# Kernel optimization log

Measured on AMD Instinct MI355X. Metric: run time of the kernel, lower is better.

Reference implementation:

```python
import jax, jax.numpy as jnp
import numpy as np

N, E, IN, H, G = 100000, 1600000, 64, 108, 128
N_LAYERS = 2  # hidden_dims=[108,108] -> 1 layer from hidden_dims[1:] + 1 final layer


def setup_inputs() -> dict:
    key = jax.random.key(0)
    ks = jax.random.split(key, 13)
    s = lambda fan_in: 1.0 / np.sqrt(fan_in)
    inp = {
        "nodes_feat": jax.random.normal(ks[0], (N, IN), jnp.float32),
        "edges_feat": jax.random.normal(ks[1], (E, 1), jnp.float32),
        "nodes_num_norm_sqrt": jax.random.uniform(ks[2], (N,), jnp.float32),
        "edges_num_norm_sqrt": jax.random.uniform(ks[3], (E,), jnp.float32),
        "W_emb": jax.random.uniform(ks[4], (IN, H), jnp.float32, -s(IN), s(IN)),
        "b_emb": jax.random.uniform(ks[5], (H,), jnp.float32, -s(IN), s(IN)),
        "pool_W": jax.random.uniform(ks[6], (N_LAYERS, H, H), jnp.float32, -s(H), s(H)),
        "pool_b": jax.random.uniform(ks[7], (N_LAYERS, H), jnp.float32, -s(H), s(H)),
        "app_W": jax.random.uniform(ks[8], (N_LAYERS, 2 * H, H), jnp.float32, -s(2 * H), s(2 * H)),
        "app_b": jax.random.uniform(ks[9], (N_LAYERS, H), jnp.float32, -s(2 * H), s(2 * H)),
        "src": jax.random.randint(ks[10], (E,), 0, N, jnp.int64 if jax.config.jax_enable_x64 else jnp.int32),
        "dst": jax.random.randint(ks[11], (E,), 0, N, jnp.int64 if jax.config.jax_enable_x64 else jnp.int32),
        "graph_ids": jnp.sort(jax.random.randint(ks[12], (N,), 0, G, jnp.int64 if jax.config.jax_enable_x64 else jnp.int32)),
        "n_graphs": G,
    }
    return inp


def reference(nodes_feat, edges_feat, nodes_num_norm_sqrt, edges_num_norm_sqrt,
              W_emb, b_emb, pool_W, pool_b, app_W, app_b,
              src, dst, graph_ids, n_graphs):
    n = nodes_feat.shape[0]
    # embedding_h
    h = nodes_feat @ W_emb + b_emb  # [N, H]
    # in-degree for mean aggregation (dropout = 0.0 so omitted)
    deg = jax.ops.segment_sum(jnp.ones((src.shape[0],), h.dtype), dst, num_segments=n)
    deg = jnp.maximum(deg, 1.0)[:, None]  # [N, 1]
    for i in range(pool_W.shape[0]):
        h_in = h
        # meanpool aggregator: per-message linear+ReLU == per-node transform then gather
        z = jax.nn.relu(h @ pool_W[i] + pool_b[i])  # [N, H]
        c = jax.ops.segment_sum(z[src], dst, num_segments=n) / deg  # mean over neighbors
        # NodeApply: linear(concat(h, c)) -> L2 normalize -> activation
        b = jnp.concatenate([h, c], axis=1) @ app_W[i] + app_b[i]
        b = b / jnp.maximum(jnp.linalg.norm(b, axis=1, keepdims=True), 1e-12)
        h = h_in + jax.nn.relu(b)  # residual (dims match: 108 == 108)
    # dgl.mean_nodes readout per graph
    cnt = jax.ops.segment_sum(jnp.ones((n,), h.dtype), graph_ids, num_segments=n_graphs)
    hg = jax.ops.segment_sum(h, graph_ids, num_segments=n_graphs) / jnp.maximum(cnt, 1.0)[:, None]
    return hg  # [n_graphs, H]
```

## Files before the change

kernel.cpp:

```cpp
#include <hip/hip_runtime.h>

#define HDIM 108
constexpr int G_GRAPHS = 128;
constexpr int MAXNB = 1024;
constexpr int CAP = 2560;

typedef _Float16 half8 __attribute__((ext_vector_type(8)));
typedef _Float16 half4v __attribute__((ext_vector_type(4)));
typedef float floatx4 __attribute__((ext_vector_type(4)));
typedef float floatx2 __attribute__((ext_vector_type(2)));

__device__ inline unsigned char f32_to_fp8(float t) {
#if __has_builtin(__builtin_amdgcn_cvt_pk_fp8_f32)
  return (unsigned char)(__builtin_amdgcn_cvt_pk_fp8_f32(t, t, 0, false) & 0xFF);
#else
  t = fminf(t, 448.f);
  if (t < 0.015625f) return (unsigned char)__float2int_rn(t * 512.f);
  unsigned u = __float_as_uint(t);
  unsigned lsb = (u >> 20) & 1;
  u += 0x7FFFFu + lsb;
  int e = (int)((u >> 23) & 0xFF) - 127;
  if (e > 8) return 0x7E;
  return (unsigned char)(((e + 7) << 3) | ((u >> 20) & 7));
#endif
}

template <bool HI>
__device__ inline floatx2 fp8x2_to_f32(unsigned v) {
#if __has_builtin(__builtin_amdgcn_cvt_pk_f32_fp8)
  return __builtin_amdgcn_cvt_pk_f32_fp8((int)v, HI);
#else
  unsigned b0 = HI ? ((v >> 16) & 0xFF) : (v & 0xFF);
  unsigned b1 = HI ? ((v >> 24) & 0xFF) : ((v >> 8) & 0xFF);
  floatx2 r;
  {
    unsigned s = b0 >> 7, e = (b0 >> 3) & 0xF, m = b0 & 7;
    float f = (e == 0) ? (float)m * 0.001953125f
                       : __uint_as_float(((e + 120u) << 23) | (m << 20));
    r[0] = s ? -f : f;
  }
  {
    unsigned s = b1 >> 7, e = (b1 >> 3) & 0xF, m = b1 & 7;
    float f = (e == 0) ? (float)m * 0.001953125f
                       : __uint_as_float(((e + 120u) << 23) | (m << 20));
    r[1] = s ? -f : f;
  }
  return r;
#endif
}

__global__ __launch_bounds__(256) void k_cvtall(const float* __restrict__ W_emb,
                                                const float* __restrict__ pool_W,
                                                const float* __restrict__ app_W,
                                                _Float16* __restrict__ wte,
                                                _Float16* __restrict__ wtp,
                                                _Float16* __restrict__ wta) {
  int idx = blockIdx.x * 256 + threadIdx.x;
  if (idx >= 86016) return;
  const float* src;
  _Float16* dst;
  int Kpad, K, split, rel;
  if (idx < 7168)       { rel = idx;          src = W_emb;            dst = wte;              Kpad = 64;  K = 64;  split = 0; }
  else if (idx < 21504) { rel = idx - 7168;   src = pool_W;           dst = wtp;              Kpad = 128; K = 108; split = 0; }
  else if (idx < 35840) { rel = idx - 21504;  src = pool_W + 11664;   dst = wtp + 14336;      Kpad = 128; K = 108; split = 0; }
  else if (idx < 60928) { rel = idx - 35840;  src = app_W;            dst = wta;              Kpad = 224; K = 216; split = 1; }
  else                  { rel = idx - 60928;  src = app_W + 23328;    dst = wta + 25088;      Kpad = 224; K = 216; split = 1; }
  int n = rel / Kpad, k = rel - n * Kpad;
  int ks;
  if (split) ks = (k < 108) ? k : (k >= 112 && k < 220) ? (k - 4) : -1;
  else       ks = (k < K) ? k : -1;
  float v = (n < 108 && ks >= 0) ? src[ks * 108 + n] : 0.f;
  dst[rel] = (_Float16)v;
}

__global__ __launch_bounds__(1024) void k_scatter(const int* __restrict__ src, const int* __restrict__ dst,
                                                  int* __restrict__ gcur, int* __restrict__ ebuf,
                                                  int E, int nb) {
  __shared__ int hist[MAXNB];
  const int tid = threadIdx.x;
  const int e0 = blockIdx.x * 16384;
  for (int b = tid; b < nb; b += 1024) hist[b] = 0;
  __syncthreads();
#pragma unroll
  for (int it = 0; it < 16; it++) {
    int e = e0 + it * 1024 + tid;
    if (e < E) atomicAdd(&hist[dst[e] >> 7], 1);
  }
  __syncthreads();
  for (int b = tid; b < nb; b += 1024) {
    int h = hist[b];
    hist[b] = h ? atomicAdd(&gcur[b * 16], h) : 0;
  }
  __syncthreads();
#pragma unroll
  for (int it = 0; it < 16; it++) {
    int e = e0 + it * 1024 + tid;
    if (e < E) {
      int d = dst[e];
      int b = d >> 7;
      int rank = atomicAdd(&hist[b], 1);
      if (rank < CAP) ebuf[(size_t)b * CAP + rank] = src[e] | ((d & 127) << 20);
    }
  }
}

__global__ __launch_bounds__(1024) void k_bagg(const unsigned char* __restrict__ z, const int* __restrict__ ebuf,
                                               const int* __restrict__ gcur, _Float16* __restrict__ c16,
                                               int N, int nb) {
  __shared__ int cnts[128];
  __shared__ int scanb[128];
  __shared__ int off[129];
  __shared__ int ecur[128];
  __shared__ int esrc[CAP];
  const int tid = threadIdx.x;
  const int b = blockIdx.x;
  const int v0 = b << 7;
  int cntb = gcur[b * 16];
  if (cntb > CAP) cntb = CAP;
  const int* eb = ebuf + (size_t)b * CAP;

  if (tid < 128) cnts[tid] = 0;
  __syncthreads();
  for (int i = tid; i < cntb; i += 1024) atomicAdd(&cnts[eb[i] >> 20], 1);
  __syncthreads();
  if (tid < 128) scanb[tid] = cnts[tid];
  __syncthreads();
#pragma unroll
  for (int st = 1; st < 128; st <<= 1) {
    int v = 0;
    if (tid < 128 && tid >= st) v = scanb[tid - st];
    __syncthreads();
    if (tid < 128) scanb[tid] += v;
    __syncthreads();
  }
  if (tid == 0) off[0] = 0;
  if (tid < 128) {
    off[tid + 1] = scanb[tid];
    ecur[tid] = scanb[tid] - cnts[tid];
  }
  __syncthreads();
  for (int i = tid; i < cntb; i += 1024) {
    int e = eb[i];
    int p = atomicAdd(&ecur[e >> 20], 1);
    esrc[p] = e & 0xFFFFF;
  }
  __syncthreads();

  const int lane = tid & 31;
  const int grp = tid >> 5;
  if (lane >= 28) return;
  const unsigned char* __restrict__ zl = z + lane * 4;
#pragma unroll 1
  for (int r = grp; r < 128; r += 32) {
    int v = v0 + r;
    if (v >= N) continue;
    int s = off[r], e2 = off[r + 1];
    float a0 = 0.f, a1 = 0.f, a2 = 0.f, a3 = 0.f;
    int j = s;
    for (; j + 4 <= e2; j += 4) {
      unsigned q0 = *(const unsigned*)(zl + (size_t)esrc[j] * 112);
      unsigned q1 = *(const unsigned*)(zl + (size_t)esrc[j + 1] * 112);
      unsigned q2 = *(const unsigned*)(zl + (size_t)esrc[j + 2] * 112);
      unsigned q3 = *(const unsigned*)(zl + (size_t)esrc[j + 3] * 112);
      floatx2 l0 = fp8x2_to_f32<false>(q0), h0 = fp8x2_to_f32<true>(q0);
      floatx2 l1 = fp8x2_to_f32<false>(q1), h1 = fp8x2_to_f32<true>(q1);
      floatx2 l2 = fp8x2_to_f32<false>(q2), h2 = fp8x2_to_f32<true>(q2);
      floatx2 l3 = fp8x2_to_f32<false>(q3), h3 = fp8x2_to_f32<true>(q3);
      a0 += (l0[0] + l1[0]) + (l2[0] + l3[0]);
      a1 += (l0[1] + l1[1]) + (l2[1] + l3[1]);
      a2 += (h0[0] + h1[0]) + (h2[0] + h3[0]);
      a3 += (h0[1] + h1[1]) + (h2[1] + h3[1]);
    }
    for (; j < e2; j++) {
      unsigned q0 = *(const unsigned*)(zl + (size_t)esrc[j] * 112);
      floatx2 l0 = fp8x2_to_f32<false>(q0), h0 = fp8x2_to_f32<true>(q0);
      a0 += l0[0]; a1 += l0[1]; a2 += h0[0]; a3 += h0[1];
    }
    int d = e2 - s;
    float inv = 1.f / (float)(d > 0 ? d : 1);
    half4v r4;
    r4[0] = (_Float16)(a0 * inv); r4[1] = (_Float16)(a1 * inv);
    r4[2] = (_Float16)(a2 * inv); r4[3] = (_Float16)(a3 * inv);
    *(half4v*)(c16 + (size_t)v * 112 + lane * 4) = r4;
  }
}

template <int KCH, int MODE>
__global__ __launch_bounds__(256, 2) void k_mmf(const void* Asrc, const _Float16* __restrict__ c16,
                                                const _Float16* __restrict__ Wt, const float* __restrict__ bias,
                                                void* outp, int N) {
  constexpr int KW = KCH * 32;
  __shared__ _Float16 As[128 * 40];
  __shared__ _Float16 Ws[112 * 40];

  const int tid = threadIdx.x;
  const int wave = tid >> 6;
  const int lane = tid & 63;
  const int lo = lane & 15;
  const int quad = lane >> 4;
  const int n0 = blockIdx.x * 128;
  const _Float16* h16 = (const _Float16*)Asrc;
  const float* feat = (const float*)Asrc;

  floatx4 acc[2][7];
#pragma unroll
  for (int rt = 0; rt < 2; rt++)
#pragma unroll
    for (int ct = 0; ct < 7; ct++) {
      floatx4 zz = {0.f, 0.f, 0.f, 0.f};
      acc[rt][ct] = zz;
    }

#pragma unroll 1
  for (int kc = 0; kc < KCH; kc++) {
#pragma unroll
    for (int it = 0; it < 2; it++) {
      int idx = tid + it * 256;
      int r = idx >> 2, sg = idx & 3;
      int gn = n0 + r;
      int k = kc * 32 + sg * 8;
      half8 v = {0, 0, 0, 0, 0, 0, 0, 0};
      if (gn < N) {
        if (MODE == 0) {
          float4 f0 = *(const float4*)(feat + (size_t)gn * 64 + k);
          float4 f1 = *(const float4*)(feat + (size_t)gn * 64 + k + 4);
          v[0] = (_Float16)f0.x; v[1] = (_Float16)f0.y; v[2] = (_Float16)f0.z; v[3] = (_Float16)f0.w;
          v[4] = (_Float16)f1.x; v[5] = (_Float16)f1.y; v[6] = (_Float16)f1.z; v[7] = (_Float16)f1.w;
        } else if (MODE == 2) {
          const _Float16* sp = (k < 112) ? (h16 + (size_t)gn * 112 + k)
                                         : (c16 + (size_t)gn * 112 + (k - 112));
          v = *(const half8*)sp;
        } else {
          if (k < 112) v = *(const half8*)(h16 + (size_t)gn * 112 + k);
        }
      }
      *(half8*)&As[r * 40 + sg * 8] = v;
    }
#pragma unroll
    for (int it = 0; it < 2; it++) {
      int idx = tid + it * 256;
      if (idx < 112 * 4) {
        int nrow = idx >> 2, sg = idx & 3;
        half8 v = *(const half8*)(Wt + (size_t)nrow * KW + kc * 32 + sg * 8);
        *(half8*)&Ws[nrow * 40 + sg * 8] = v;
      }
    }
    __syncthreads();

    half8 a0 = *(const half8*)&As[(wave * 32 + lo) * 40 + quad * 8];
    half8 a1 = *(const half8*)&As[(wave * 32 + 16 + lo) * 40 + quad * 8];
#pragma unroll
    for (int ct = 0; ct < 7; ct++) {
      half8 b = *(const half8*)&Ws[(ct * 16 + lo) * 40 + quad * 8];
      acc[0][ct] = __builtin_amdgcn_mfma_f32_16x16x32_f16(a0, b, acc[0][ct], 0, 0, 0);
      acc[1][ct] = __builtin_amdgcn_mfma_f32_16x16x32_f16(a1, b, acc[1][ct], 0, 0, 0);
    }
    __syncthreads();
  }

  float bias_v[7];
#pragma unroll
  for (int ct = 0; ct < 7; ct++) {
    int col = ct * 16 + lo;
    bias_v[ct] = (col < 108) ? bias[col] : 0.f;
  }

  if (MODE == 2) {
    _Float16* out16 = (_Float16*)outp;
#pragma unroll
    for (int rt = 0; rt < 2; rt++) {
#pragma unroll
      for (int reg = 0; reg < 4; reg++) {
        int gr = n0 + wave * 32 + rt * 16 + quad * 4 + reg;
        float bv[7];
        float ssq = 0.f;
#pragma unroll
        for (int ct = 0; ct < 7; ct++) {
          float t = acc[rt][ct][reg] + bias_v[ct];
          bv[ct] = t;
          ssq += t * t;
        }
#pragma unroll
        for (int s = 1; s < 16; s <<= 1) ssq += __shfl_xor(ssq, s, 16);
        float scale = 1.f / fmaxf(sqrtf(ssq), 1e-12f);
        if (gr < N) {
          _Float16* hp = out16 + (size_t)gr * 112 + lo;
#pragma unroll
          for (int ct = 0; ct < 7; ct++) {
            float hv = (float)hp[ct * 16];
            hp[ct * 16] = (_Float16)(hv + fmaxf(bv[ct] * scale, 0.f));
          }
        }
      }
    }
  } else if (MODE == 1) {
    unsigned char* outb = (unsigned char*)outp;
#pragma unroll
    for (int rt = 0; rt < 2; rt++) {
#pragma unroll
      for (int reg = 0; reg < 4; reg++) {
        int gr = n0 + wave * 32 + rt * 16 + quad * 4 + reg;
        if (gr < N) {
          unsigned char* op = outb + (size_t)gr * 112 + lo;
#pragma unroll
          for (int ct = 0; ct < 7; ct++) {
            float t = fmaxf(acc[rt][ct][reg] + bias_v[ct], 0.f);
            op[ct * 16] = f32_to_fp8(t);
          }
        }
      }
    }
  } else {
    _Float16* out16 = (_Float16*)outp;
#pragma unroll
    for (int rt = 0; rt < 2; rt++) {
#pragma unroll
      for (int reg = 0; reg < 4; reg++) {
        int gr = n0 + wave * 32 + rt * 16 + quad * 4 + reg;
        if (gr < N) {
          _Float16* op = out16 + (size_t)gr * 112 + lo;
#pragma unroll
          for (int ct = 0; ct < 7; ct++) {
            float t = acc[rt][ct][reg] + bias_v[ct];
            op[ct * 16] = (_Float16)t;
          }
        }
      }
    }
  }
}

__global__ __launch_bounds__(256) void k_readout(const _Float16* __restrict__ h, const int* __restrict__ gid,
                                                 float* __restrict__ hg, int N) {
  const int CH = 64;
  const int lane = threadIdx.x & 31;
  const int grp = threadIdx.x >> 5;
  int start = (blockIdx.x * 8 + grp) * CH;
  if (start >= N || lane >= 27) return;
  int end = min(start + CH, N);
  float a0 = 0.f, a1 = 0.f, a2 = 0.f, a3 = 0.f;
  int cur = gid[start];
  for (int i = start; i < end; i++) {
    int g = gid[i];
    if (g != cur) {
      float* base = &hg[(size_t)cur * HDIM + lane * 4];
      atomicAdd(base + 0, a0); atomicAdd(base + 1, a1);
      atomicAdd(base + 2, a2); atomicAdd(base + 3, a3);
      a0 = a1 = a2 = a3 = 0.f;
      cur = g;
    }
    half4v v = *(const half4v*)(h + (size_t)i * 112 + lane * 4);
    a0 += (float)v[0]; a1 += (float)v[1]; a2 += (float)v[2]; a3 += (float)v[3];
  }
  float* base = &hg[(size_t)cur * HDIM + lane * 4];
  atomicAdd(base + 0, a0); atomicAdd(base + 1, a1);
  atomicAdd(base + 2, a2); atomicAdd(base + 3, a3);
}

__global__ __launch_bounds__(256) void k_div(const float* __restrict__ hg, const int* __restrict__ gid,
                                             float* __restrict__ out, int total, int N) {
  int i = blockIdx.x * 256 + threadIdx.x;
  if (i < total) {
    int g = i / HDIM;
    int lo = 0, hi = N;
    while (lo < hi) { int m = (lo + hi) >> 1; if (gid[m] < g) lo = m + 1; else hi = m; }
    int lb = lo;
    lo = 0; hi = N;
    while (lo < hi) { int m = (lo + hi) >> 1; if (gid[m] <= g) lo = m + 1; else hi = m; }
    int c = lo - lb;
    out[i] = hg[i] / (float)(c > 0 ? c : 1);
  }
}

extern "C" void kernel_launch(void* const* d_in, const int* in_sizes, int n_in,
                              void* d_out, int out_size, void* d_ws, size_t ws_size,
                              hipStream_t stream) {
  (void)n_in; (void)ws_size; (void)out_size;
  const float* nodes_feat = (const float*)d_in[0];
  const float* W_emb = (const float*)d_in[4];
  const float* b_emb = (const float*)d_in[5];
  const float* pool_W = (const float*)d_in[6];
  const float* pool_b = (const float*)d_in[7];
  const float* app_W = (const float*)d_in[8];
  const float* app_b = (const float*)d_in[9];
  const int* src = (const int*)d_in[10];
  const int* dst = (const int*)d_in[11];
  const int* gid = (const int*)d_in[12];
  const int N = in_sizes[2];
  const int E = in_sizes[10];
  float* out = (float*)d_out;

  const int nb = (N + 127) >> 7;

  char* ws = (char*)d_ws;
  size_t off = 0;
  auto alloc = [&](size_t bytes) -> size_t {
    size_t o = off;
    off += (bytes + 1023) & ~size_t(1023);
    return o;
  };
  size_t o_gcur = alloc((size_t)MAXNB * 16 * 4);
  size_t o_hg   = alloc((size_t)G_GRAPHS * HDIM * 4);
  size_t zero_bytes = off;
  size_t o_ebuf = alloc((size_t)MAXNB * CAP * 4);
  size_t o_h  = alloc((size_t)N * 112 * 2);
  size_t o_z  = alloc((size_t)N * 112);
  size_t o_c  = alloc((size_t)N * 112 * 2);
  size_t o_we = alloc((size_t)112 * 64 * 2);
  size_t o_wp = alloc((size_t)2 * 112 * 128 * 2);
  size_t o_wa = alloc((size_t)2 * 112 * 224 * 2);

  int*           gcur = (int*)(ws + o_gcur);
  float*         hg   = (float*)(ws + o_hg);
  int*           ebuf = (int*)(ws + o_ebuf);
  _Float16*      h16  = (_Float16*)(ws + o_h);
  unsigned char* z8   = (unsigned char*)(ws + o_z);
  _Float16*      c16  = (_Float16*)(ws + o_c);
  _Float16*      wte  = (_Float16*)(ws + o_we);
  _Float16*      wtp  = (_Float16*)(ws + o_wp);
  _Float16*      wta  = (_Float16*)(ws + o_wa);

  (void)hipMemsetAsync(d_ws, 0, zero_bytes, stream);

  k_cvtall<<<(86016 + 255) / 256, 256, 0, stream>>>(W_emb, pool_W, app_W, wte, wtp, wta);

  k_scatter<<<(E + 16383) / 16384, 1024, 0, stream>>>(src, dst, gcur, ebuf, E, nb);

  const int nbMM = (N + 127) / 128;
  k_mmf<2, 0><<<nbMM, 256, 0, stream>>>(nodes_feat, nullptr, wte, b_emb, h16, N);

  for (int i = 0; i < 2; i++) {
    k_mmf<4, 1><<<nbMM, 256, 0, stream>>>(h16, nullptr, wtp + i * 112 * 128,
                                          pool_b + i * HDIM, z8, N);
    k_bagg<<<nb, 1024, 0, stream>>>(z8, ebuf, gcur, c16, N, nb);
    k_mmf<7, 2><<<nbMM, 256, 0, stream>>>(h16, c16, wta + i * 112 * 224,
                                          app_b + i * HDIM, h16, N);
  }

  k_readout<<<(N + 8 * 64 - 1) / (8 * 64), 256, 0, stream>>>(h16, gid, hg, N);
  k_div<<<(G_GRAPHS * HDIM + 255) / 256, 256, 0, stream>>>(hg, gid, out, G_GRAPHS * HDIM, N);
}
```

Measured before the change: 348.6 us.

## Fuse weight conversion into scatter, halve GEMM row tile, pad fp8 rows to 128

Weight fp16 conversion moves into the first threads of the scatter kernel, which removes one kernel launch. The node-GEMM kernels now use 64-row tiles with one 16-row MFMA strip per wave instead of 128 rows, which doubles the grid and lowers register pressure. The fp8 z buffer stride grows from 112 to 128 bytes so gathered rows in the aggregation are aligned to cache lines. The cost is less weight reuse per block in the GEMM and a larger z buffer.

```diff
diff --git a/kernel.cpp b/kernel.cpp
--- a/kernel.cpp
+++ b/kernel.cpp
@@ -49,36 +49,37 @@
 #endif
 }
 
-__global__ __launch_bounds__(256) void k_cvtall(const float* __restrict__ W_emb,
-                                                const float* __restrict__ pool_W,
-                                                const float* __restrict__ app_W,
-                                                _Float16* __restrict__ wte,
-                                                _Float16* __restrict__ wtp,
-                                                _Float16* __restrict__ wta) {
-  int idx = blockIdx.x * 256 + threadIdx.x;
-  if (idx >= 86016) return;
-  const float* src;
-  _Float16* dst;
-  int Kpad, K, split, rel;
-  if (idx < 7168)       { rel = idx;          src = W_emb;            dst = wte;              Kpad = 64;  K = 64;  split = 0; }
-  else if (idx < 21504) { rel = idx - 7168;   src = pool_W;           dst = wtp;              Kpad = 128; K = 108; split = 0; }
-  else if (idx < 35840) { rel = idx - 21504;  src = pool_W + 11664;   dst = wtp + 14336;      Kpad = 128; K = 108; split = 0; }
-  else if (idx < 60928) { rel = idx - 35840;  src = app_W;            dst = wta;              Kpad = 224; K = 216; split = 1; }
-  else                  { rel = idx - 60928;  src = app_W + 23328;    dst = wta + 25088;      Kpad = 224; K = 216; split = 1; }
-  int n = rel / Kpad, k = rel - n * Kpad;
-  int ks;
-  if (split) ks = (k < 108) ? k : (k >= 112 && k < 220) ? (k - 4) : -1;
-  else       ks = (k < K) ? k : -1;
-  float v = (n < 108 && ks >= 0) ? src[ks * 108 + n] : 0.f;
-  dst[rel] = (_Float16)v;
-}
-
 __global__ __launch_bounds__(1024) void k_scatter(const int* __restrict__ src, const int* __restrict__ dst,
                                                   int* __restrict__ gcur, int* __restrict__ ebuf,
+                                                  const float* __restrict__ W_emb,
+                                                  const float* __restrict__ pool_W,
+                                                  const float* __restrict__ app_W,
+                                                  _Float16* __restrict__ wte,
+                                                  _Float16* __restrict__ wtp,
+                                                  _Float16* __restrict__ wta,
                                                   int E, int nb) {
   __shared__ int hist[MAXNB];
   const int tid = threadIdx.x;
   const int e0 = blockIdx.x * 16384;
+
+  int gi = blockIdx.x * 1024 + tid;
+  if (gi < 86016) {
+    const float* srcw;
+    _Float16* dstw;
+    int Kpad, K, split, rel;
+    if (gi < 7168)       { rel = gi;          srcw = W_emb;          dstw = wte;         Kpad = 64;  K = 64;  split = 0; }
+    else if (gi < 21504) { rel = gi - 7168;   srcw = pool_W;         dstw = wtp;         Kpad = 128; K = 108; split = 0; }
+    else if (gi < 35840) { rel = gi - 21504;  srcw = pool_W + 11664; dstw = wtp + 14336; Kpad = 128; K = 108; split = 0; }
+    else if (gi < 60928) { rel = gi - 35840;  srcw = app_W;          dstw = wta;         Kpad = 224; K = 216; split = 1; }
+    else                 { rel = gi - 60928;  srcw = app_W + 23328;  dstw = wta + 25088; Kpad = 224; K = 216; split = 1; }
+    int n = rel / Kpad, k = rel - n * Kpad;
+    int ks;
+    if (split) ks = (k < 108) ? k : (k >= 112 && k < 220) ? (k - 4) : -1;
+    else       ks = (k < K) ? k : -1;
+    float v = (n < 108 && ks >= 0) ? srcw[ks * 108 + n] : 0.f;
+    dstw[rel] = (_Float16)v;
+  }
+
   for (int b = tid; b < nb; b += 1024) hist[b] = 0;
   __syncthreads();
 #pragma unroll
@@ -158,10 +159,10 @@
     float a0 = 0.f, a1 = 0.f, a2 = 0.f, a3 = 0.f;
     int j = s;
     for (; j + 4 <= e2; j += 4) {
-      unsigned q0 = *(const unsigned*)(zl + (size_t)esrc[j] * 112);
-      unsigned q1 = *(const unsigned*)(zl + (size_t)esrc[j + 1] * 112);
-      unsigned q2 = *(const unsigned*)(zl + (size_t)esrc[j + 2] * 112);
-      unsigned q3 = *(const unsigned*)(zl + (size_t)esrc[j + 3] * 112);
+      unsigned q0 = *(const unsigned*)(zl + (size_t)esrc[j] * 128);
+      unsigned q1 = *(const unsigned*)(zl + (size_t)esrc[j + 1] * 128);
+      unsigned q2 = *(const unsigned*)(zl + (size_t)esrc[j + 2] * 128);
+      unsigned q3 = *(const unsigned*)(zl + (size_t)esrc[j + 3] * 128);
       floatx2 l0 = fp8x2_to_f32<false>(q0), h0 = fp8x2_to_f32<true>(q0);
       floatx2 l1 = fp8x2_to_f32<false>(q1), h1 = fp8x2_to_f32<true>(q1);
       floatx2 l2 = fp8x2_to_f32<false>(q2), h2 = fp8x2_to_f32<true>(q2);
@@ -172,7 +173,7 @@
       a3 += (h0[1] + h1[1]) + (h2[1] + h3[1]);
     }
     for (; j < e2; j++) {
-      unsigned q0 = *(const unsigned*)(zl + (size_t)esrc[j] * 112);
+      unsigned q0 = *(const unsigned*)(zl + (size_t)esrc[j] * 128);
       floatx2 l0 = fp8x2_to_f32<false>(q0), h0 = fp8x2_to_f32<true>(q0);
       a0 += l0[0]; a1 += l0[1]; a2 += h0[0]; a3 += h0[1];
     }
@@ -186,11 +187,11 @@
 }
 
 template <int KCH, int MODE>
-__global__ __launch_bounds__(256, 2) void k_mmf(const void* Asrc, const _Float16* __restrict__ c16,
-                                                const _Float16* __restrict__ Wt, const float* __restrict__ bias,
-                                                void* outp, int N) {
+__global__ __launch_bounds__(256) void k_mmf(const void* Asrc, const _Float16* __restrict__ c16,
+                                             const _Float16* __restrict__ Wt, const float* __restrict__ bias,
+                                             void* outp, int N) {
   constexpr int KW = KCH * 32;
-  __shared__ _Float16 As[128 * 40];
+  __shared__ _Float16 As[64 * 40];
   __shared__ _Float16 Ws[112 * 40];
 
   const int tid = threadIdx.x;
@@ -198,25 +199,21 @@
   const int lane = tid & 63;
   const int lo = lane & 15;
   const int quad = lane >> 4;
-  const int n0 = blockIdx.x * 128;
+  const int n0 = blockIdx.x * 64;
   const _Float16* h16 = (const _Float16*)Asrc;
   const float* feat = (const float*)Asrc;
 
-  floatx4 acc[2][7];
-#pragma unroll
-  for (int rt = 0; rt < 2; rt++)
-#pragma unroll
-    for (int ct = 0; ct < 7; ct++) {
-      floatx4 zz = {0.f, 0.f, 0.f, 0.f};
-      acc[rt][ct] = zz;
-    }
+  floatx4 acc[7];
+#pragma unroll
+  for (int ct = 0; ct < 7; ct++) {
+    floatx4 zz = {0.f, 0.f, 0.f, 0.f};
+    acc[ct] = zz;
+  }
 
 #pragma unroll 1
   for (int kc = 0; kc < KCH; kc++) {
-#pragma unroll
-    for (int it = 0; it < 2; it++) {
-      int idx = tid + it * 256;
-      int r = idx >> 2, sg = idx & 3;
+    {
+      int r = tid >> 2, sg = tid & 3;
       int gn = n0 + r;
       int k = kc * 32 + sg * 8;
       half8 v = {0, 0, 0, 0, 0, 0, 0, 0};
@@ -239,7 +236,7 @@
 #pragma unroll
     for (int it = 0; it < 2; it++) {
       int idx = tid + it * 256;
-      if (idx < 112 * 4) {
+      if (idx < 448) {
         int nrow = idx >> 2, sg = idx & 3;
         half8 v = *(const half8*)(Wt + (size_t)nrow * KW + kc * 32 + sg * 8);
         *(half8*)&Ws[nrow * 40 + sg * 8] = v;
@@ -247,13 +244,11 @@
     }
     __syncthreads();
 
-    half8 a0 = *(const half8*)&As[(wave * 32 + lo) * 40 + quad * 8];
-    half8 a1 = *(const half8*)&As[(wave * 32 + 16 + lo) * 40 + quad * 8];
+    half8 a = *(const half8*)&As[(wave * 16 + lo) * 40 + quad * 8];
 #pragma unroll
     for (int ct = 0; ct < 7; ct++) {
       half8 b = *(const half8*)&Ws[(ct * 16 + lo) * 40 + quad * 8];
-      acc[0][ct] = __builtin_amdgcn_mfma_f32_16x16x32_f16(a0, b, acc[0][ct], 0, 0, 0);
-      acc[1][ct] = __builtin_amdgcn_mfma_f32_16x16x32_f16(a1, b, acc[1][ct], 0, 0, 0);
+      acc[ct] = __builtin_amdgcn_mfma_f32_16x16x32_f16(a, b, acc[ct], 0, 0, 0);
     }
     __syncthreads();
   }
@@ -268,62 +263,53 @@
   if (MODE == 2) {
     _Float16* out16 = (_Float16*)outp;
 #pragma unroll
-    for (int rt = 0; rt < 2; rt++) {
-#pragma unroll
-      for (int reg = 0; reg < 4; reg++) {
-        int gr = n0 + wave * 32 + rt * 16 + quad * 4 + reg;
-        float bv[7];
-        float ssq = 0.f;
+    for (int reg = 0; reg < 4; reg++) {
+      int gr = n0 + wave * 16 + quad * 4 + reg;
+      float bv[7];
+      float ssq = 0.f;
+#pragma unroll
+      for (int ct = 0; ct < 7; ct++) {
+        float t = acc[ct][reg] + bias_v[ct];
+        bv[ct] = t;
+        ssq += t * t;
+      }
+#pragma unroll
+      for (int s = 1; s < 16; s <<= 1) ssq += __shfl_xor(ssq, s, 16);
+      float scale = 1.f / fmaxf(sqrtf(ssq), 1e-12f);
+      if (gr < N) {
+        _Float16* hp = out16 + (size_t)gr * 112 + lo;
 #pragma unroll
         for (int ct = 0; ct < 7; ct++) {
-          float t = acc[rt][ct][reg] + bias_v[ct];
-          bv[ct] = t;
-          ssq += t * t;
-        }
-#pragma unroll
-        for (int s = 1; s < 16; s <<= 1) ssq += __shfl_xor(ssq, s, 16);
-        float scale = 1.f / fmaxf(sqrtf(ssq), 1e-12f);
-        if (gr < N) {
-          _Float16* hp = out16 + (size_t)gr * 112 + lo;
-#pragma unroll
-          for (int ct = 0; ct < 7; ct++) {
-            float hv = (float)hp[ct * 16];
-            hp[ct * 16] = (_Float16)(hv + fmaxf(bv[ct] * scale, 0.f));
-          }
+          float hv = (float)hp[ct * 16];
+          hp[ct * 16] = (_Float16)(hv + fmaxf(bv[ct] * scale, 0.f));
         }
       }
     }
   } else if (MODE == 1) {
     unsigned char* outb = (unsigned char*)outp;
 #pragma unroll
-    for (int rt = 0; rt < 2; rt++) {
-#pragma unroll
-      for (int reg = 0; reg < 4; reg++) {
-        int gr = n0 + wave * 32 + rt * 16 + quad * 4 + reg;
-        if (gr < N) {
-          unsigned char* op = outb + (size_t)gr * 112 + lo;
-#pragma unroll
-          for (int ct = 0; ct < 7; ct++) {
-            float t = fmaxf(acc[rt][ct][reg] + bias_v[ct], 0.f);
-            op[ct * 16] = f32_to_fp8(t);
-          }
+    for (int reg = 0; reg < 4; reg++) {
+      int gr = n0 + wave * 16 + quad * 4 + reg;
+      if (gr < N) {
+        unsigned char* op = outb + (size_t)gr * 128 + lo;
+#pragma unroll
+        for (int ct = 0; ct < 7; ct++) {
+          float t = fmaxf(acc[ct][reg] + bias_v[ct], 0.f);
+          op[ct * 16] = f32_to_fp8(t);
         }
       }
     }
   } else {
     _Float16* out16 = (_Float16*)outp;
 #pragma unroll
-    for (int rt = 0; rt < 2; rt++) {
-#pragma unroll
-      for (int reg = 0; reg < 4; reg++) {
-        int gr = n0 + wave * 32 + rt * 16 + quad * 4 + reg;
-        if (gr < N) {
-          _Float16* op = out16 + (size_t)gr * 112 + lo;
-#pragma unroll
-          for (int ct = 0; ct < 7; ct++) {
-            float t = acc[rt][ct][reg] + bias_v[ct];
-            op[ct * 16] = (_Float16)t;
-          }
+    for (int reg = 0; reg < 4; reg++) {
+      int gr = n0 + wave * 16 + quad * 4 + reg;
+      if (gr < N) {
+        _Float16* op = out16 + (size_t)gr * 112 + lo;
+#pragma unroll
+        for (int ct = 0; ct < 7; ct++) {
+          float t = acc[ct][reg] + bias_v[ct];
+          op[ct * 16] = (_Float16)t;
         }
       }
     }
@@ -404,7 +390,7 @@
   size_t zero_bytes = off;
   size_t o_ebuf = alloc((size_t)MAXNB * CAP * 4);
   size_t o_h  = alloc((size_t)N * 112 * 2);
-  size_t o_z  = alloc((size_t)N * 112);
+  size_t o_z  = alloc((size_t)N * 128);
   size_t o_c  = alloc((size_t)N * 112 * 2);
   size_t o_we = alloc((size_t)112 * 64 * 2);
   size_t o_wp = alloc((size_t)2 * 112 * 128 * 2);
@@ -422,18 +408,18 @@
 
   (void)hipMemsetAsync(d_ws, 0, zero_bytes, stream);
 
-  k_cvtall<<<(86016 + 255) / 256, 256, 0, stream>>>(W_emb, pool_W, app_W, wte, wtp, wta);
-
-  k_scatter<<<(E + 16383) / 16384, 1024, 0, stream>>>(src, dst, gcur, ebuf, E, nb);
-
-  const int nbMM = (N + 127) / 128;
+  k_scatter<<<(E + 16383) / 16384, 1024, 0, stream>>>(src, dst, gcur, ebuf,
+                                                      W_emb, pool_W, app_W,
+                                                      wte, wtp, wta, E, nb);
+
+  const int nbMM = (N + 63) / 64;
   k_mmf<2, 0><<<nbMM, 256, 0, stream>>>(nodes_feat, nullptr, wte, b_emb, h16, N);
 
   for (int i = 0; i < 2; i++) {
-    k_mmf<4, 1><<<nbMM, 256, 0, stream>>>(h16, nullptr, wtp + i * 112 * 128,
+    k_mmf<4, 1><<<nbMM, 256, 0, stream>>>(h16, nullptr, wtp + i * 14336,
                                           pool_b + i * HDIM, z8, N);
     k_bagg<<<nb, 1024, 0, stream>>>(z8, ebuf, gcur, c16, N, nb);
-    k_mmf<7, 2><<<nbMM, 256, 0, stream>>>(h16, c16, wta + i * 112 * 224,
+    k_mmf<7, 2><<<nbMM, 256, 0, stream>>>(h16, c16, wta + i * 25088,
                                           app_b + i * HDIM, h16, N);
   }
 
```

Result: faster. 337.3 us (-3.2%).
